# Kernel tuning notes

Hardware: AMD Instinct MI355X
Metric: run time of the kernel (lower is better)

The kernel has to match this reference:

```python
import jax, jax.numpy as jnp
import numpy as np

N = 100000  # nodes


def setup_inputs() -> dict:
    key = jax.random.key(0)
    k0, k1, k2, k3 = jax.random.split(key, 4)
    IN, H, OUT = 256, 256, 128  # in_channels, 2*out_channels, out_channels
    E = 1600000
    x = jax.random.normal(k0, (N, IN), dtype=jnp.float32)
    edge_index = jax.random.randint(k1, (2, E), 0, N, dtype=jnp.int32)
    W1 = jax.random.normal(k2, (IN, H), dtype=jnp.float32) / np.sqrt(IN)
    b1 = jnp.zeros((H,), dtype=jnp.float32)
    W2 = jax.random.normal(k3, (H, OUT), dtype=jnp.float32) / np.sqrt(H)
    b2 = jnp.zeros((OUT,), dtype=jnp.float32)
    return {"x": x, "edge_index": edge_index, "W1": W1, "b1": b1, "W2": W2, "b2": b2}


def _gcn_layer(x, W, b, src, dst, norm):
    # PyG GCNConv: out[i] = sum_{(j->i)} norm_e * (x @ W)[j] + b, over A + I
    h = x @ W
    msg = h[src] * norm[:, None]          # [E+N, F] gathered edge messages
    out = jax.ops.segment_sum(msg, dst, num_segments=N)
    return out + b


def reference(x, edge_index, W1, b1, W2, b2):
    src, dst = edge_index[0], edge_index[1]
    loop = jnp.arange(N, dtype=src.dtype)
    src = jnp.concatenate([src, loop])    # add self-loops
    dst = jnp.concatenate([dst, loop])
    # symmetric normalization: deg computed on target (col) with unit weights
    deg = jax.ops.segment_sum(jnp.ones_like(dst, dtype=x.dtype), dst, num_segments=N)
    dinv = jnp.where(deg > 0, jax.lax.rsqrt(deg), 0.0)
    norm = dinv[src] * dinv[dst]
    h = jax.nn.relu(_gcn_layer(x, W1, b1, src, dst, norm))
    out = jax.nn.relu(_gcn_layer(h, W2, b2, src, dst, norm))
    return out
```

## Files before the change

kernel.cpp:

```cpp
#include <hip/hip_runtime.h>
#include <hip/hip_fp16.h>


typedef _Float16 f16x8 __attribute__((ext_vector_type(8)));
typedef float f32x4 __attribute__((ext_vector_type(4)));

constexpr int CAP = 64;


__device__ inline void pack_w_body(const float* __restrict__ W, __half* __restrict__ Wp,
                                   int NC, int t) {
    const int NT = NC / 16;
    int lane = t & 63;
    int rest = t >> 6;
    int nt = rest % NT;
    int ks = rest / NT;
    int n = nt * 16 + (lane & 15);
    int k0 = ks * 32 + (lane >> 4) * 8;
    __half tmp[8];
#pragma unroll
    for (int j = 0; j < 8; ++j) tmp[j] = __float2half_rn(W[(size_t)(k0 + j) * NC + n]);
    ((uint4*)Wp)[t] = *(const uint4*)tmp;
}

__global__ __launch_bounds__(256) void prep_kernel(const int* __restrict__ src,
                                                   const int* __restrict__ dst, int E,
                                                   int* __restrict__ cnt,
                                                   int* __restrict__ colFixed,
                                                   const float* __restrict__ x,
                                                   __half* __restrict__ xh, int n8,
                                                   const float* __restrict__ W1,
                                                   __half* __restrict__ Wp1,
                                                   const float* __restrict__ W2,
                                                   __half* __restrict__ Wp2,
                                                   int nbFill, int nbPack) {
    const int b = blockIdx.x;
    const int tid = threadIdx.x;
    if (b < nbFill) {
        int e = b * 256 + tid;
        if (e < E) {
            int d = dst[e];
            int slot = atomicAdd(&cnt[d], 1);
            if (slot < CAP) colFixed[(size_t)d * CAP + slot] = src[e];
        }
    } else if (b < nbFill + nbPack) {
        int i = (b - nbFill) * 256 + tid;
        if (i < n8) {
            float4 a = ((const float4*)x)[(size_t)i * 2];
            float4 bb = ((const float4*)x)[(size_t)i * 2 + 1];
            __half2 h[4];
            h[0] = __floats2half2_rn(a.x, a.y);
            h[1] = __floats2half2_rn(a.z, a.w);
            h[2] = __floats2half2_rn(bb.x, bb.y);
            h[3] = __floats2half2_rn(bb.z, bb.w);
            ((uint4*)xh)[i] = *(const uint4*)h;
        }
    } else if (b < nbFill + nbPack + 32) {
        int t = (b - nbFill - nbPack) * 256 + tid;
        pack_w_body(W1, Wp1, 256, t);
    } else {
        int t = (b - nbFill - nbPack - 32) * 256 + tid;
        pack_w_body(W2, Wp2, 128, t);
    }
}

__global__ __launch_bounds__(256) void aggregate256_h(const __half* __restrict__ xh,
                                                      const int* __restrict__ cnt,
                                                      const int* __restrict__ colFixed,
                                                      __half* __restrict__ out, int N) {
    const int lane = threadIdx.x & 63;
    const int i = blockIdx.x * 4 + (threadIdx.x >> 6);
    if (i >= N) return;
    const int degt = cnt[i];
    const float di = rsqrtf((float)(degt + 1));
    const int deg = (degt < CAP) ? degt : CAP;
    const uint2* __restrict__ hv = (const uint2*)xh;
    uint2 raw = hv[(size_t)i * 64 + lane];
    float2 f0 = __half22float2(*(const __half2*)&raw.x);
    float2 f1 = __half22float2(*(const __half2*)&raw.y);
    float ax = di * f0.x, ay = di * f0.y, az = di * f1.x, aw = di * f1.y;
    const int* __restrict__ cl = colFixed + (size_t)i * CAP;
    int e = 0;
    for (; e + 8 <= deg; e += 8) {
        int s[8];
#pragma unroll
        for (int j = 0; j < 8; ++j) s[j] = cl[e + j];
        float w[8];
#pragma unroll
        for (int j = 0; j < 8; ++j) w[j] = rsqrtf((float)(cnt[s[j]] + 1));
        uint2 u[8];
#pragma unroll
        for (int j = 0; j < 8; ++j) u[j] = hv[(size_t)s[j] * 64 + lane];
#pragma unroll
        for (int j = 0; j < 8; ++j) {
            float2 g0 = __half22float2(*(const __half2*)&u[j].x);
            float2 g1 = __half22float2(*(const __half2*)&u[j].y);
            ax = fmaf(w[j], g0.x, ax);
            ay = fmaf(w[j], g0.y, ay);
            az = fmaf(w[j], g1.x, az);
            aw = fmaf(w[j], g1.y, aw);
        }
    }
    for (; e < deg; ++e) {
        int s = cl[e];
        float w = rsqrtf((float)(cnt[s] + 1));
        uint2 u = hv[(size_t)s * 64 + lane];
        float2 g0 = __half22float2(*(const __half2*)&u.x);
        float2 g1 = __half22float2(*(const __half2*)&u.y);
        ax = fmaf(w, g0.x, ax);
        ay = fmaf(w, g0.y, ay);
        az = fmaf(w, g1.x, az);
        aw = fmaf(w, g1.y, aw);
    }
    __half2 h0 = __floats2half2_rn(ax * di, ay * di);
    __half2 h1 = __floats2half2_rn(az * di, aw * di);
    uint2 o;
    o.x = *(const unsigned int*)&h0;
    o.y = *(const unsigned int*)&h1;
    ((uint2*)out)[(size_t)i * 64 + lane] = o;
}

__global__ __launch_bounds__(256) void gemm_mfma256(const __half* __restrict__ A,
                                                    const __half* __restrict__ Wp,
                                                    const float* __restrict__ bias,
                                                    __half* __restrict__ out, int M) {
    constexpr int NT = 16;
    const int lane = threadIdx.x & 63;
    const int wave = threadIdx.x >> 6;
    const int kg = lane >> 4;
    const int row = blockIdx.x * 64 + wave * 16 + (lane & 15);
    const int rowc = (row < M) ? row : (M - 1);

    f32x4 acc[NT];
#pragma unroll
    for (int nt = 0; nt < NT; ++nt) acc[nt] = {0.f, 0.f, 0.f, 0.f};

    const f16x8* __restrict__ Ap = (const f16x8*)(A + (size_t)rowc * 256 + kg * 8);
    const f16x8* __restrict__ Wf = (const f16x8*)Wp;

#pragma unroll
    for (int ks = 0; ks < 8; ++ks) {
        f16x8 xfrag = Ap[ks * 4];
        const f16x8* wrow = Wf + (size_t)(ks * NT) * 64 + lane;
#pragma unroll
        for (int nt = 0; nt < NT; ++nt) {
            f16x8 wfrag = wrow[nt * 64];
            acc[nt] = __builtin_amdgcn_mfma_f32_16x16x32_f16(wfrag, xfrag, acc[nt], 0, 0, 0);
        }
    }

    if (row < M) {
#pragma unroll
        for (int nt = 0; nt < NT; ++nt) {
            const int n0 = nt * 16 + kg * 4;
            f32x4 v = acc[nt];
            float4 bb = *(const float4*)(bias + n0);
            v[0] = fmaxf(v[0] + bb.x, 0.f);
            v[1] = fmaxf(v[1] + bb.y, 0.f);
            v[2] = fmaxf(v[2] + bb.z, 0.f);
            v[3] = fmaxf(v[3] + bb.w, 0.f);
            __half2 h0 = __floats2half2_rn(v[0], v[1]);
            __half2 h1 = __floats2half2_rn(v[2], v[3]);
            uint2 o;
            o.x = *(const unsigned int*)&h0;
            o.y = *(const unsigned int*)&h1;
            *(uint2*)(out + (size_t)row * 256 + n0) = o;
        }
    }
}

__global__ __launch_bounds__(256) void gemm_mfma128(const __half* __restrict__ A,
                                                    const __half* __restrict__ Wp,
                                                    const int* __restrict__ cnt,
                                                    __half* __restrict__ out, int M) {
    constexpr int NT = 8;
    const int lane = threadIdx.x & 63;
    const int wave = threadIdx.x >> 6;
    const int kg = lane >> 4;
    const int row = blockIdx.x * 64 + wave * 16 + (lane & 15);
    const int rowc = (row < M) ? row : (M - 1);

    f32x4 acc[NT];
#pragma unroll
    for (int nt = 0; nt < NT; ++nt) acc[nt] = {0.f, 0.f, 0.f, 0.f};

    const f16x8* __restrict__ Ap = (const f16x8*)(A + (size_t)rowc * 256 + kg * 8);
    const f16x8* __restrict__ Wf = (const f16x8*)Wp;

#pragma unroll
    for (int ks = 0; ks < 8; ++ks) {
        f16x8 xfrag = Ap[ks * 4];
        const f16x8* wrow = Wf + (size_t)(ks * NT) * 64 + lane;
#pragma unroll
        for (int nt = 0; nt < NT; ++nt) {
            f16x8 wfrag = wrow[nt * 64];
            acc[nt] = __builtin_amdgcn_mfma_f32_16x16x32_f16(wfrag, xfrag, acc[nt], 0, 0, 0);
        }
    }

    if (row < M) {
        float rs = rsqrtf((float)(cnt[row] + 1));
#pragma unroll
        for (int nt = 0; nt < NT; ++nt) {
            const int n0 = nt * 16 + kg * 4;
            f32x4 v = acc[nt];
            __half2 h0 = __floats2half2_rn(v[0] * rs, v[1] * rs);
            __half2 h1 = __floats2half2_rn(v[2] * rs, v[3] * rs);
            uint2 o;
            o.x = *(const unsigned int*)&h0;
            o.y = *(const unsigned int*)&h1;
            *(uint2*)(out + (size_t)row * 128 + n0) = o;
        }
    }
}

__global__ __launch_bounds__(256) void aggregate128_h_bias_relu(const __half* __restrict__ h,
                                                                const int* __restrict__ cnt,
                                                                const int* __restrict__ colFixed,
                                                                const float* __restrict__ bias,
                                                                float* __restrict__ out, int N) {
    const int lane = threadIdx.x & 63;
    const int i = blockIdx.x * 4 + (threadIdx.x >> 6);
    if (i >= N) return;
    const int degt = cnt[i];
    const float di = rsqrtf((float)(degt + 1));
    const int deg = (degt < CAP) ? degt : CAP;
    const unsigned int* __restrict__ hv = (const unsigned int*)h;
    float2 v = __half22float2(*(const __half2*)&hv[(size_t)i * 64 + lane]);
    float ax = v.x, ay = v.y;
    const int* __restrict__ cl = colFixed + (size_t)i * CAP;
    int e = 0;
    for (; e + 8 <= deg; e += 8) {
        int s[8];
#pragma unroll
        for (int j = 0; j < 8; ++j) s[j] = cl[e + j];
        unsigned int u[8];
#pragma unroll
        for (int j = 0; j < 8; ++j) u[j] = hv[(size_t)s[j] * 64 + lane];
#pragma unroll
        for (int j = 0; j < 8; ++j) {
            float2 g = __half22float2(*(const __half2*)&u[j]);
            ax += g.x;
            ay += g.y;
        }
    }
    for (; e < deg; ++e) {
        float2 g = __half22float2(*(const __half2*)&hv[(size_t)cl[e] * 64 + lane]);
        ax += g.x;
        ay += g.y;
    }
    float2 bb = ((const float2*)bias)[lane];
    float2 r;
    r.x = fmaxf(fmaf(ax, di, bb.x), 0.f);
    r.y = fmaxf(fmaf(ay, di, bb.y), 0.f);
    ((float2*)out)[(size_t)i * 64 + lane] = r;
}

extern "C" void kernel_launch(void* const* d_in, const int* in_sizes, int n_in,
                              void* d_out, int out_size, void* d_ws, size_t ws_size,
                              hipStream_t stream) {
    const float* x  = (const float*)d_in[0];
    const int*   ei = (const int*)d_in[1];
    const float* W1 = (const float*)d_in[2];
    const float* b1 = (const float*)d_in[3];
    const float* W2 = (const float*)d_in[4];
    const float* b2 = (const float*)d_in[5];
    float* out = (float*)d_out;

    const int N = in_sizes[0] / 256;
    const int E = in_sizes[1] / 2;
    const int* src = ei;
    const int* dst = ei + E;

    char* ws = (char*)d_ws;
    size_t off = 0;
    auto alloc = [&](size_t bytes) -> char* {
        char* p = ws + off;
        off += (bytes + 255) & ~(size_t)255;
        return p;
    };
    int*    cnt      = (int*)alloc((size_t)N * 4);
    int*    colFixed = (int*)alloc((size_t)N * CAP * 4);
    __half* Wp1      = (__half*)alloc((size_t)256 * 256 * 2);
    __half* Wp2      = (__half*)alloc((size_t)256 * 128 * 2);
    __half* bufA     = (__half*)alloc((size_t)N * 256 * 2);
    __half* bufB     = (__half*)alloc((size_t)N * 256 * 2);
    __half* xh    = bufA;
    __half* h1h   = bufA;
    __half* buf1h = bufB;
    __half* buf2h = bufB;

    hipMemsetAsync(cnt, 0, (size_t)N * 4, stream);

    const int n8 = (N * 256) / 8;
    const int nbFill = (E + 255) / 256;
    const int nbPack = (n8 + 255) / 256;
    const int nbPrep = nbFill + nbPack + 32 + 16;
    prep_kernel<<<nbPrep, 256, 0, stream>>>(src, dst, E, cnt, colFixed, x, xh, n8,
                                            W1, Wp1, W2, Wp2, nbFill, nbPack);

    const int AB = (N + 3) / 4;
    const int GB = (N + 63) / 64;

    aggregate256_h<<<AB, 256, 0, stream>>>(xh, cnt, colFixed, buf1h, N);
    gemm_mfma256<<<GB, 256, 0, stream>>>(buf1h, Wp1, b1, h1h, N);
    gemm_mfma128<<<GB, 256, 0, stream>>>(h1h, Wp2, cnt, buf2h, N);
    aggregate128_h_bias_relu<<<AB, 256, 0, stream>>>(buf2h, cnt, colFixed, b2, out, N);
}
```

Measured before the change: 446.6 us.

## Fuse both GEMMs into one kernel, re-fragmenting activations via wave shuffles

Merges the first GEMM (with bias and ReLU) and the second GEMM into a single kernel. The intermediate 256-wide hidden activations stay in registers as fp16 and are redistributed into MFMA input-fragment layout with cross-lane shuffles, so they are never written to or re-read from global memory. This removes one kernel launch and about 100 MB of intermediate traffic. The cost is higher register pressure, since two accumulator sets are live, plus extra shuffle instructions. Either could lower occupancy.

```diff
diff --git a/kernel.cpp b/kernel.cpp
--- a/kernel.cpp
+++ b/kernel.cpp
@@ -120,90 +120,91 @@
     ((uint2*)out)[(size_t)i * 64 + lane] = o;
 }
 
-__global__ __launch_bounds__(256) void gemm_mfma256(const __half* __restrict__ A,
-                                                    const __half* __restrict__ Wp,
-                                                    const float* __restrict__ bias,
+__global__ __launch_bounds__(256) void gemm_fused12(const __half* __restrict__ A,
+                                                    const __half* __restrict__ Wp1,
+                                                    const float* __restrict__ bias1,
+                                                    const __half* __restrict__ Wp2,
+                                                    const int* __restrict__ cnt,
                                                     __half* __restrict__ out, int M) {
-    constexpr int NT = 16;
     const int lane = threadIdx.x & 63;
     const int wave = threadIdx.x >> 6;
     const int kg = lane >> 4;
-    const int row = blockIdx.x * 64 + wave * 16 + (lane & 15);
+    const int r = lane & 15;
+    const int row = blockIdx.x * 64 + wave * 16 + r;
     const int rowc = (row < M) ? row : (M - 1);
 
-    f32x4 acc[NT];
-#pragma unroll
-    for (int nt = 0; nt < NT; ++nt) acc[nt] = {0.f, 0.f, 0.f, 0.f};
+    f32x4 acc1[16];
+#pragma unroll
+    for (int nt = 0; nt < 16; ++nt) acc1[nt] = {0.f, 0.f, 0.f, 0.f};
 
     const f16x8* __restrict__ Ap = (const f16x8*)(A + (size_t)rowc * 256 + kg * 8);
-    const f16x8* __restrict__ Wf = (const f16x8*)Wp;
-
+    const f16x8* __restrict__ Wf1 = (const f16x8*)Wp1;
 #pragma unroll
     for (int ks = 0; ks < 8; ++ks) {
         f16x8 xfrag = Ap[ks * 4];
-        const f16x8* wrow = Wf + (size_t)(ks * NT) * 64 + lane;
-#pragma unroll
-        for (int nt = 0; nt < NT; ++nt) {
+        const f16x8* wrow = Wf1 + (size_t)(ks * 16) * 64 + lane;
+#pragma unroll
+        for (int nt = 0; nt < 16; ++nt) {
             f16x8 wfrag = wrow[nt * 64];
-            acc[nt] = __builtin_amdgcn_mfma_f32_16x16x32_f16(wfrag, xfrag, acc[nt], 0, 0, 0);
-        }
-    }
-
-    if (row < M) {
-#pragma unroll
-        for (int nt = 0; nt < NT; ++nt) {
-            const int n0 = nt * 16 + kg * 4;
-            f32x4 v = acc[nt];
-            float4 bb = *(const float4*)(bias + n0);
-            v[0] = fmaxf(v[0] + bb.x, 0.f);
-            v[1] = fmaxf(v[1] + bb.y, 0.f);
-            v[2] = fmaxf(v[2] + bb.z, 0.f);
-            v[3] = fmaxf(v[3] + bb.w, 0.f);
-            __half2 h0 = __floats2half2_rn(v[0], v[1]);
-            __half2 h1 = __floats2half2_rn(v[2], v[3]);
-            uint2 o;
-            o.x = *(const unsigned int*)&h0;
-            o.y = *(const unsigned int*)&h1;
-            *(uint2*)(out + (size_t)row * 256 + n0) = o;
-        }
-    }
-}
-
-__global__ __launch_bounds__(256) void gemm_mfma128(const __half* __restrict__ A,
-                                                    const __half* __restrict__ Wp,
-                                                    const int* __restrict__ cnt,
-                                                    __half* __restrict__ out, int M) {
-    constexpr int NT = 8;
-    const int lane = threadIdx.x & 63;
-    const int wave = threadIdx.x >> 6;
-    const int kg = lane >> 4;
-    const int row = blockIdx.x * 64 + wave * 16 + (lane & 15);
-    const int rowc = (row < M) ? row : (M - 1);
-
-    f32x4 acc[NT];
-#pragma unroll
-    for (int nt = 0; nt < NT; ++nt) acc[nt] = {0.f, 0.f, 0.f, 0.f};
-
-    const f16x8* __restrict__ Ap = (const f16x8*)(A + (size_t)rowc * 256 + kg * 8);
-    const f16x8* __restrict__ Wf = (const f16x8*)Wp;
-
+            acc1[nt] = __builtin_amdgcn_mfma_f32_16x16x32_f16(wfrag, xfrag, acc1[nt], 0, 0, 0);
+        }
+    }
+
+    unsigned int hw[32];
+#pragma unroll
+    for (int nt = 0; nt < 16; ++nt) {
+        float4 bb = *(const float4*)(bias1 + nt * 16 + kg * 4);
+        f32x4 v = acc1[nt];
+        v[0] = fmaxf(v[0] + bb.x, 0.f);
+        v[1] = fmaxf(v[1] + bb.y, 0.f);
+        v[2] = fmaxf(v[2] + bb.z, 0.f);
+        v[3] = fmaxf(v[3] + bb.w, 0.f);
+        __half2 h0 = __floats2half2_rn(v[0], v[1]);
+        __half2 h1 = __floats2half2_rn(v[2], v[3]);
+        hw[nt * 2 + 0] = *(const unsigned int*)&h0;
+        hw[nt * 2 + 1] = *(const unsigned int*)&h1;
+    }
+
+    const int a = kg >> 1;
+    const int b = kg & 1;
+    const int p0 = r + 32 * b;
+    const int p1 = p0 + 16;
+
+    f32x4 acc2[8];
+#pragma unroll
+    for (int nt = 0; nt < 8; ++nt) acc2[nt] = {0.f, 0.f, 0.f, 0.f};
+
+    const f16x8* __restrict__ Wf2 = (const f16x8*)Wp2;
 #pragma unroll
     for (int ks = 0; ks < 8; ++ks) {
-        f16x8 xfrag = Ap[ks * 4];
-        const f16x8* wrow = Wf + (size_t)(ks * NT) * 64 + lane;
-#pragma unroll
-        for (int nt = 0; nt < NT; ++nt) {
+        unsigned int lo0 = (unsigned int)__shfl((int)hw[4 * ks + 0], p0, 64);
+        unsigned int lo1 = (unsigned int)__shfl((int)hw[4 * ks + 1], p0, 64);
+        unsigned int lo2 = (unsigned int)__shfl((int)hw[4 * ks + 2], p0, 64);
+        unsigned int lo3 = (unsigned int)__shfl((int)hw[4 * ks + 3], p0, 64);
+        unsigned int hi0 = (unsigned int)__shfl((int)hw[4 * ks + 0], p1, 64);
+        unsigned int hi1 = (unsigned int)__shfl((int)hw[4 * ks + 1], p1, 64);
+        unsigned int hi2 = (unsigned int)__shfl((int)hw[4 * ks + 2], p1, 64);
+        unsigned int hi3 = (unsigned int)__shfl((int)hw[4 * ks + 3], p1, 64);
+        unsigned int xf[4];
+        xf[0] = a ? lo2 : lo0;
+        xf[1] = a ? lo3 : lo1;
+        xf[2] = a ? hi2 : hi0;
+        xf[3] = a ? hi3 : hi1;
+        f16x8 xfrag = *(const f16x8*)xf;
+        const f16x8* wrow = Wf2 + (size_t)(ks * 8) * 64 + lane;
+#pragma unroll
+        for (int nt = 0; nt < 8; ++nt) {
             f16x8 wfrag = wrow[nt * 64];
-            acc[nt] = __builtin_amdgcn_mfma_f32_16x16x32_f16(wfrag, xfrag, acc[nt], 0, 0, 0);
+            acc2[nt] = __builtin_amdgcn_mfma_f32_16x16x32_f16(wfrag, xfrag, acc2[nt], 0, 0, 0);
         }
     }
 
     if (row < M) {
         float rs = rsqrtf((float)(cnt[row] + 1));
 #pragma unroll
-        for (int nt = 0; nt < NT; ++nt) {
+        for (int nt = 0; nt < 8; ++nt) {
             const int n0 = nt * 16 + kg * 4;
-            f32x4 v = acc[nt];
+            f32x4 v = acc2[nt];
             __half2 h0 = __floats2half2_rn(v[0] * rs, v[1] * rs);
             __half2 h1 = __floats2half2_rn(v[2] * rs, v[3] * rs);
             uint2 o;
@@ -286,9 +287,8 @@
     __half* bufA     = (__half*)alloc((size_t)N * 256 * 2);
     __half* bufB     = (__half*)alloc((size_t)N * 256 * 2);
     __half* xh    = bufA;
-    __half* h1h   = bufA;
+    __half* buf2h = bufA;
     __half* buf1h = bufB;
-    __half* buf2h = bufB;
 
     hipMemsetAsync(cnt, 0, (size_t)N * 4, stream);
 
@@ -303,7 +303,6 @@
     const int GB = (N + 63) / 64;
 
     aggregate256_h<<<AB, 256, 0, stream>>>(xh, cnt, colFixed, buf1h, N);
-    gemm_mfma256<<<GB, 256, 0, stream>>>(buf1h, Wp1, b1, h1h, N);
-    gemm_mfma128<<<GB, 256, 0, stream>>>(h1h, Wp2, cnt, buf2h, N);
+    gemm_fused12<<<GB, 256, 0, stream>>>(buf1h, Wp1, b1, Wp2, cnt, buf2h, N);
     aggregate128_h_bias_relu<<<AB, 256, 0, stream>>>(buf2h, cnt, colFixed, b2, out, N);
 }
```

Measured after the change: 465.0 us. +4.1%, slower.
